# Performance work log

Measured on AMD Instinct MI355X. Metric: run time of the kernel, lower is better.

## Reference

```python
import jax, jax.numpy as jnp
import numpy as np

B, D_IN, P, H, E, K, NS, OUT = 4096, 512, 1024, 2048, 8, 2, 2, 29
HS = H * NS  # shared-expert intermediate size


def setup_inputs() -> dict:
    key = jax.random.key(0)
    ks = jax.random.split(key, 20)
    g = lambda i, shape, fan: jax.random.normal(ks[i], shape, jnp.float32) * (1.0 / np.sqrt(fan))
    return {
        "x": jax.random.normal(ks[0], (B, D_IN), jnp.float32),
        # input projection
        "Wproj": g(1, (D_IN, P), D_IN), "bproj": jnp.zeros((P,), jnp.float32),
        # router (Tutel top gate: linear, no bias)
        "Wg": g(2, (P, E), P),
        # fine experts (grouped FFN with fc1/fc2 bias)
        "W1": g(3, (E, P, H), P), "b1": jnp.zeros((E, H), jnp.float32),
        "W2": g(4, (E, H, P), H), "b2": jnp.zeros((E, P), jnp.float32),
        # shared experts: DeepseekV3MLP (SwiGLU with bias)
        "sg_w": g(5, (P, HS), P), "sg_b": jnp.zeros((HS,), jnp.float32),
        "su_w": g(6, (P, HS), P), "su_b": jnp.zeros((HS,), jnp.float32),
        "sd_w": g(7, (HS, P), HS), "sd_b": jnp.zeros((P,), jnp.float32),
        # output MLP + head
        "m1_w": g(8, (P, H), P), "m1_b": jnp.zeros((H,), jnp.float32),
        "m2_w": g(9, (H, H), H), "m2_b": jnp.zeros((H,), jnp.float32),
        "head_w": g(10, (H, OUT), H), "head_b": jnp.zeros((OUT,), jnp.float32),
    }


def reference(x, Wproj, bproj, Wg, W1, b1, W2, b2,
              sg_w, sg_b, su_w, su_b, sd_w, sd_b,
              m1_w, m1_b, m2_w, m2_b, head_w, head_b):
    silu = jax.nn.silu
    # input projection  [B, P]
    p = x @ Wproj + bproj

    # --- Tutel-style top-k gating (inference: gate_noise = 0, normalize=True) ---
    probs = jax.nn.softmax(p @ Wg, axis=-1)               # [B, E]
    top_vals, top_idx = jax.lax.top_k(probs, K)           # [B, K]
    gates = top_vals / jnp.sum(top_vals, axis=-1, keepdims=True)
    # combine weights as dense [B, E] (zero for non-selected experts)
    combine = jnp.zeros((p.shape[0], E), p.dtype).at[
        jnp.arange(p.shape[0])[:, None], top_idx].add(gates)

    # --- grouped-GEMM experts (ffn with fc1/fc2 bias, silu) ---
    h = silu(jnp.einsum('bp,eph->beh', p, W1) + b1)       # [B, E, H]
    eo = jnp.einsum('beh,ehp->bep', h, W2) + b2           # [B, E, P]
    moe_out = jnp.einsum('be,bep->bp', combine, eo)       # weighted combine

    # --- shared experts: SwiGLU MLP on residual stream ---
    shared = (silu(p @ sg_w + sg_b) * (p @ su_w + su_b)) @ sd_w + sd_b
    combined = moe_out + shared

    # --- output MLP + head ---
    hid = silu(combined @ m1_w + m1_b) @ m2_w + m2_b
    return hid @ head_w + head_b
```

## Files before the change

kernel.cpp:

```cpp
#include <hip/hip_runtime.h>
#include <hip/hip_bf16.h>
#include <cstdint>

typedef unsigned short us;
typedef __attribute__((ext_vector_type(4))) float f32x4;
typedef __attribute__((ext_vector_type(8))) short bf16x8;
typedef __attribute__((ext_vector_type(4))) short s16x4;
typedef __attribute__((ext_vector_type(8))) short s16x8;

__device__ __forceinline__ float b2f(us s){
  union { float f; unsigned u; } x; x.u = ((unsigned)s) << 16; return x.f;
}
__device__ __forceinline__ us f2b(float f){
  union { float f; unsigned u; } x; x.f = f;
  unsigned r = x.u + 0x7FFFu + ((x.u >> 16) & 1u);
  return (us)(r >> 16);
}

#define GLDS16(gp, lp) __builtin_amdgcn_global_load_lds( \
    (const __attribute__((address_space(1))) void*)(gp), \
    (__attribute__((address_space(3))) void*)(lp), 16, 0, 0)

__global__ void detect_kernel(const unsigned* __restrict__ xw, int* __restrict__ flag){
  __shared__ int cnt;
  if (threadIdx.x == 0) cnt = 0;
  __syncthreads();
  int c = 0;
  for (int i = threadIdx.x; i < 1024; i += 256){
    const unsigned e = (xw[i] >> 7) & 0xFF;
    if (e >= 100 && e <= 140) ++c;
  }
  atomicAdd(&cnt, c);
  __syncthreads();
  if (threadIdx.x == 0) *flag = (cnt < 512) ? 1 : 0;
}

template<bool OUT_BF16, bool SILU, bool MULG>
__global__ __launch_bounds__(256, 2)
void gemm_plain(const us* __restrict__ A, int lda,
                const us* __restrict__ BT, int ldb,
                void* __restrict__ Cout, int ldc,
                const us* __restrict__ bias,
                const us* __restrict__ mulg,
                int M, int N, int K, int Nvalid)
{
  __shared__ us As[128*32];
  __shared__ us Bs[128*32];
  const int bm = blockIdx.y * 128, bn = blockIdx.x * 128;
  const int tid = threadIdx.x, wave = tid >> 6, lane = tid & 63;
  const int llo = lane & 15, lhi = lane >> 4;

  const us* aP[2]; const us* bP[2]; us* lA[2]; us* lB[2];
#pragma unroll
  for (int s = 0; s < 2; ++s){
    const int chunk = s*256 + wave*64 + lane;
    const int r = chunk >> 2, cc = chunk & 3;
    aP[s] = A  + (size_t)(bm + r) * lda + cc*8;
    bP[s] = BT + (size_t)(bn + r) * ldb + cc*8;
    lA[s] = As + (size_t)(s*256 + wave*64) * 8;
    lB[s] = Bs + (size_t)(s*256 + wave*64) * 8;
  }

  f32x4 acc[4][4] = {};
  const int waveM = (wave >> 1) * 64, waveN = (wave & 1) * 64;

  for (int k0 = 0; k0 < K; k0 += 32){
    GLDS16(aP[0] + k0, lA[0]);
    GLDS16(aP[1] + k0, lA[1]);
    GLDS16(bP[0] + k0, lB[0]);
    GLDS16(bP[1] + k0, lB[1]);
    __syncthreads();
    bf16x8 af[4], bv[4];
#pragma unroll
    for (int t = 0; t < 4; ++t){
      af[t] = *reinterpret_cast<const bf16x8*>(As + (waveM + t*16 + llo)*32 + lhi*8);
      bv[t] = *reinterpret_cast<const bf16x8*>(Bs + (waveN + t*16 + llo)*32 + lhi*8);
    }
#pragma unroll
    for (int mt = 0; mt < 4; ++mt)
#pragma unroll
      for (int nt = 0; nt < 4; ++nt)
        acc[mt][nt] = __builtin_amdgcn_mfma_f32_16x16x32_bf16(af[mt], bv[nt], acc[mt][nt], 0, 0, 0);
    __syncthreads();
  }

#pragma unroll
  for (int nt = 0; nt < 4; ++nt){
    const int col = bn + waveN + nt*16 + llo;
    float bb = 0.f;
    if (bias && col < Nvalid) bb = b2f(bias[col]);
#pragma unroll
    for (int mt = 0; mt < 4; ++mt){
      const int row0 = bm + waveM + mt*16 + lhi*4;
#pragma unroll
      for (int r = 0; r < 4; ++r){
        if (col < Nvalid){
          float v = acc[mt][nt][r] + bb;
          if (SILU) v = v / (1.f + __expf(-v));
          if (MULG) v *= b2f(mulg[(size_t)(row0 + r) * ldc + col]);
          if (OUT_BF16) ((us*)Cout)[(size_t)(row0 + r) * ldc + col] = f2b(v);
          else          ((float*)Cout)[(size_t)(row0 + r) * ldc + col] = v;
        }
      }
    }
  }
}

template<bool OUT_BF16, bool SILU>
__global__ __launch_bounds__(256, 2)
void gemm_group(const us* __restrict__ Abase, int lda,
                const int* __restrict__ rowmap,
                const int* __restrict__ offsets,
                const us* __restrict__ BTbase,
                void* __restrict__ Cout, int ldc,
                const us* __restrict__ biasbase,
                int N, int K)
{
  const int e   = blockIdx.z;
  const int off = offsets[e];
  const int Te  = offsets[e + 1] - off;
  const int bmL = blockIdx.y * 128;
  if (bmL >= Te) return;

  __shared__ us As[128*32];
  __shared__ us Bs[128*32];
  const us* BT   = BTbase  + (size_t)e * N * K;
  const us* bias = biasbase + (size_t)e * N;
  const int bn = blockIdx.x * 128;
  const int tid = threadIdx.x, wave = tid >> 6, lane = tid & 63;
  const int llo = lane & 15, lhi = lane >> 4;

  const us* aP[2]; const us* bP[2]; us* lA[2]; us* lB[2];
#pragma unroll
  for (int s = 0; s < 2; ++s){
    const int chunk = s*256 + wave*64 + lane;
    const int r = chunk >> 2, cc = chunk & 3;
    int pos = off + bmL + r; if (pos > 8191) pos = 8191;
    const int arow = rowmap ? rowmap[pos] : pos;
    aP[s] = Abase + (size_t)arow * lda + cc*8;
    bP[s] = BT + (size_t)(bn + r) * K + cc*8;
    lA[s] = As + (size_t)(s*256 + wave*64) * 8;
    lB[s] = Bs + (size_t)(s*256 + wave*64) * 8;
  }

  f32x4 acc[4][4] = {};
  const int waveM = (wave >> 1) * 64, waveN = (wave & 1) * 64;

  for (int k0 = 0; k0 < K; k0 += 32){
    GLDS16(aP[0] + k0, lA[0]);
    GLDS16(aP[1] + k0, lA[1]);
    GLDS16(bP[0] + k0, lB[0]);
    GLDS16(bP[1] + k0, lB[1]);
    __syncthreads();
    bf16x8 af[4], bv[4];
#pragma unroll
    for (int t = 0; t < 4; ++t){
      af[t] = *reinterpret_cast<const bf16x8*>(As + (waveM + t*16 + llo)*32 + lhi*8);
      bv[t] = *reinterpret_cast<const bf16x8*>(Bs + (waveN + t*16 + llo)*32 + lhi*8);
    }
#pragma unroll
    for (int mt = 0; mt < 4; ++mt)
#pragma unroll
      for (int nt = 0; nt < 4; ++nt)
        acc[mt][nt] = __builtin_amdgcn_mfma_f32_16x16x32_bf16(af[mt], bv[nt], acc[mt][nt], 0, 0, 0);
    __syncthreads();
  }

#pragma unroll
  for (int nt = 0; nt < 4; ++nt){
    const int col = bn + waveN + nt*16 + llo;
    const float bb = b2f(bias[col]);
#pragma unroll
    for (int mt = 0; mt < 4; ++mt){
      const int localBase = bmL + waveM + mt*16 + lhi*4;
#pragma unroll
      for (int r = 0; r < 4; ++r){
        const int local = localBase + r;
        if (local < Te){
          float v = acc[mt][nt][r] + bb;
          if (SILU) v = v / (1.f + __expf(-v));
          const size_t row = (size_t)(off + local);
          if (OUT_BF16) ((us*)Cout)[row * ldc + col] = f2b(v);
          else          ((float*)Cout)[row * ldc + col] = v;
        }
      }
    }
  }
}

__global__ __launch_bounds__(256, 2)
void gemm_head(const us* __restrict__ A, const us* __restrict__ BT,
               float* __restrict__ Cpart)
{
  __shared__ us As[128*32];
  __shared__ us Bs[128*32];
  const int bm = blockIdx.y * 128;
  const int koff = blockIdx.z * 256;
  const int tid = threadIdx.x, wave = tid >> 6, lane = tid & 63;
  const int llo = lane & 15, lhi = lane >> 4;

  const us* aP[2]; const us* bP[2]; us* lA[2]; us* lB[2];
#pragma unroll
  for (int s = 0; s < 2; ++s){
    const int chunk = s*256 + wave*64 + lane;
    const int r = chunk >> 2, cc = chunk & 3;
    aP[s] = A  + (size_t)(bm + r) * 2048 + koff + cc*8;
    bP[s] = BT + (size_t)r * 2048 + koff + cc*8;
    lA[s] = As + (size_t)(s*256 + wave*64) * 8;
    lB[s] = Bs + (size_t)(s*256 + wave*64) * 8;
  }

  f32x4 acc[4][4] = {};
  const int waveM = (wave >> 1) * 64, waveN = (wave & 1) * 64;

  for (int k0 = 0; k0 < 256; k0 += 32){
    GLDS16(aP[0] + k0, lA[0]);
    GLDS16(aP[1] + k0, lA[1]);
    GLDS16(bP[0] + k0, lB[0]);
    GLDS16(bP[1] + k0, lB[1]);
    __syncthreads();
    bf16x8 af[4], bv[4];
#pragma unroll
    for (int t = 0; t < 4; ++t){
      af[t] = *reinterpret_cast<const bf16x8*>(As + (waveM + t*16 + llo)*32 + lhi*8);
      bv[t] = *reinterpret_cast<const bf16x8*>(Bs + (waveN + t*16 + llo)*32 + lhi*8);
    }
#pragma unroll
    for (int mt = 0; mt < 4; ++mt)
#pragma unroll
      for (int nt = 0; nt < 4; ++nt)
        acc[mt][nt] = __builtin_amdgcn_mfma_f32_16x16x32_bf16(af[mt], bv[nt], acc[mt][nt], 0, 0, 0);
    __syncthreads();
  }

  float* out = Cpart + (size_t)blockIdx.z * 4096 * 32;
#pragma unroll
  for (int nt = 0; nt < 4; ++nt){
    const int col = waveN + nt*16 + llo;
    if (col >= 29) continue;
#pragma unroll
    for (int mt = 0; mt < 4; ++mt){
      const int row0 = bm + waveM + mt*16 + lhi*4;
#pragma unroll
      for (int r = 0; r < 4; ++r)
        out[(size_t)(row0 + r) * 32 + col] = acc[mt][nt][r];
    }
  }
}

__global__ void reduce_head(const float* __restrict__ part, const us* __restrict__ bias,
                            void* __restrict__ dst, const int* __restrict__ flag){
  const int i = blockIdx.x * 256 + threadIdx.x;
  if (i >= 4096*29) return;
  const int t = i / 29, c = i - t * 29;
  float s = b2f(bias[c]);
#pragma unroll
  for (int z = 0; z < 8; ++z) s += part[((size_t)z * 4096 + t) * 32 + c];
  if (*flag) ((float*)dst)[i] = s;
  else       ((us*)dst)[i] = f2b(s);
}

__global__ void transpose_any(const void* __restrict__ src_, us* __restrict__ dst,
                              int R, int C, long long smat, long long dmat,
                              const int* __restrict__ flag)
{
  const int f32 = *flag;
  dst += (size_t)blockIdx.z * dmat;
  __shared__ us tile[32][33];
  const int c0 = blockIdx.x * 32, r0 = blockIdx.y * 32;
  const int tx = threadIdx.x & 31, ty = threadIdx.x >> 5;
#pragma unroll
  for (int i = 0; i < 4; ++i){
    const int r = r0 + ty + i*8, c = c0 + tx;
    const size_t idx = (size_t)blockIdx.z * smat + (size_t)r * C + c;
    us v = 0;
    if (c < C){
      if (f32) v = f2b(((const float*)src_)[idx]);
      else     v = ((const us*)src_)[idx];
    }
    tile[ty + i*8][tx] = v;
  }
  __syncthreads();
#pragma unroll
  for (int i = 0; i < 4; ++i){
    const int dr = c0 + ty + i*8;
    dst[(size_t)dr * R + r0 + tx] = tile[tx][ty + i*8];
  }
}

__global__ void cvt_any_bf(const void* __restrict__ src, us* __restrict__ dst, int n,
                           const int* __restrict__ flag){
  const int i = (blockIdx.x * 256 + threadIdx.x) * 4;
  if (i >= n) return;
  s16x4 o;
  if (*flag){
    f32x4 v = *reinterpret_cast<const f32x4*>((const float*)src + i);
#pragma unroll
    for (int k = 0; k < 4; ++k) o[k] = (short)f2b(v[k]);
  } else {
    o = *reinterpret_cast<const s16x4*>((const us*)src + i);
  }
  *reinterpret_cast<s16x4*>(dst + i) = o;
}

__global__ void compose_router(const void* __restrict__ Wproj, const void* __restrict__ Wg,
                               float* __restrict__ M, const int* __restrict__ flag)
{
  const int f32 = *flag;
  const int wave = threadIdx.x >> 6, lane = threadIdx.x & 63;
  const int d = blockIdx.x * 4 + wave;
  float acc[8] = {0,0,0,0,0,0,0,0};
  for (int n = lane; n < 1024; n += 64){
    float wp;
    if (f32) wp = ((const float*)Wproj)[(size_t)d * 1024 + n];
    else     wp = b2f(((const us*)Wproj)[(size_t)d * 1024 + n]);
    if (f32){
      const float* wg = (const float*)Wg + (size_t)n * 8;
#pragma unroll
      for (int e = 0; e < 8; ++e) acc[e] += wp * wg[e];
    } else {
      const s16x8 wg = *reinterpret_cast<const s16x8*>((const us*)Wg + (size_t)n * 8);
#pragma unroll
      for (int e = 0; e < 8; ++e) acc[e] += wp * b2f((us)wg[e]);
    }
  }
#pragma unroll
  for (int e = 0; e < 8; ++e){
    float v = acc[e];
    for (int off = 32; off > 0; off >>= 1) v += __shfl_down(v, off);
    if (lane == 0) M[(size_t)d * 8 + e] = v;
  }
}

__global__ void router2(const void* __restrict__ x, const float* __restrict__ M,
                        int* __restrict__ eidx, float* __restrict__ gates,
                        const int* __restrict__ flag)
{
  const int f32 = *flag;
  const int wave = threadIdx.x >> 6, lane = threadIdx.x & 63;
  const int t = blockIdx.x * 4 + wave;
  float l[8] = {0,0,0,0,0,0,0,0};
  for (int d = lane; d < 512; d += 64){
    float xv;
    if (f32) xv = ((const float*)x)[(size_t)t * 512 + d];
    else     xv = b2f(((const us*)x)[(size_t)t * 512 + d]);
    const float* mr = M + (size_t)d * 8;
#pragma unroll
    for (int e = 0; e < 8; ++e) l[e] += xv * mr[e];
  }
#pragma unroll
  for (int e = 0; e < 8; ++e){
    float v = l[e];
    for (int off = 32; off > 0; off >>= 1) v += __shfl_down(v, off);
    l[e] = v;
  }
  if (lane == 0){
    int e0 = 0; float v0 = l[0];
#pragma unroll
    for (int e = 1; e < 8; ++e) if (l[e] > v0){ v0 = l[e]; e0 = e; }
    int e1 = (e0 == 0) ? 1 : 0; float v1 = l[e1];
#pragma unroll
    for (int e = 0; e < 8; ++e) if (e != e0 && l[e] > v1){ v1 = l[e]; e1 = e; }
    const float g1 = 1.f / (1.f + __expf(v0 - v1));
    eidx[t*2] = e0;  eidx[t*2+1] = e1;
    gates[t*2] = 1.f - g1; gates[t*2+1] = g1;
  }
}

__global__ void hist_kernel(const int* __restrict__ eidx, int* __restrict__ counts){
  __shared__ int lh[8];
  if (threadIdx.x < 8) lh[threadIdx.x] = 0;
  __syncthreads();
  const int i = blockIdx.x * 256 + threadIdx.x;
  atomicAdd(&lh[eidx[i]], 1);
  __syncthreads();
  if (threadIdx.x < 8) atomicAdd(&counts[threadIdx.x], lh[threadIdx.x]);
}

__global__ void scan_kernel(const int* __restrict__ counts, int* __restrict__ offsets){
  if (threadIdx.x == 0){
    int s = 0;
    for (int e = 0; e < 8; ++e){ offsets[e] = s; s += counts[e]; }
    offsets[8] = s;
  }
}

__global__ void fill_kernel(const int* __restrict__ eidx, const int* __restrict__ offsets,
                            int* __restrict__ fillg, int* __restrict__ pos_tk,
                            int* __restrict__ tok_of_pos){
  __shared__ int lh[8];
  __shared__ int lbase[8];
  if (threadIdx.x < 8) lh[threadIdx.x] = 0;
  __syncthreads();
  const int i = blockIdx.x * 256 + threadIdx.x;
  const int e = eidx[i];
  const int r = atomicAdd(&lh[e], 1);
  __syncthreads();
  if (threadIdx.x < 8) lbase[threadIdx.x] = atomicAdd(&fillg[threadIdx.x], lh[threadIdx.x]);
  __syncthreads();
  const int pos = offsets[e] + lbase[e] + r;
  pos_tk[i] = pos;
  tok_of_pos[pos] = i >> 1;
}

__global__ void combine_kernel(const float* __restrict__ eo, const float* __restrict__ shr,
                               const int* __restrict__ pos_tk, const float* __restrict__ gates,
                               us* __restrict__ comb){
  const int t = blockIdx.x;
  const int c = threadIdx.x * 4;
  const int p0 = pos_tk[t*2], p1 = pos_tk[t*2+1];
  const float g0 = gates[t*2], g1 = gates[t*2+1];
  f32x4 a = *reinterpret_cast<const f32x4*>(eo + (size_t)p0 * 1024 + c);
  f32x4 b = *reinterpret_cast<const f32x4*>(eo + (size_t)p1 * 1024 + c);
  f32x4 s = *reinterpret_cast<const f32x4*>(shr + (size_t)t * 1024 + c);
  s16x4 o;
#pragma unroll
  for (int k = 0; k < 4; ++k) o[k] = (short)f2b(g0 * a[k] + g1 * b[k] + s[k]);
  *reinterpret_cast<s16x4*>(comb + (size_t)t * 1024 + c) = o;
}

extern "C" void kernel_launch(void* const* d_in, const int* in_sizes, int n_in,
                              void* d_out, int out_size, void* d_ws, size_t ws_size,
                              hipStream_t stream)
{
  const void* x      = d_in[0];
  const void* Wproj  = d_in[1];
  const us*   bproj  = (const us*)d_in[2];
  const void* Wg     = d_in[3];
  const void* W1     = d_in[4];
  const us*   b1     = (const us*)d_in[5];
  const void* W2     = d_in[6];
  const us*   b2     = (const us*)d_in[7];
  const void* sg_w   = d_in[8];
  const us*   sg_b   = (const us*)d_in[9];
  const void* su_w   = d_in[10];
  const us*   su_b   = (const us*)d_in[11];
  const void* sd_w   = d_in[12];
  const us*   sd_b   = (const us*)d_in[13];
  const void* m1_w   = d_in[14];
  const us*   m1_b   = (const us*)d_in[15];
  const void* m2_w   = d_in[16];
  const us*   m2_b   = (const us*)d_in[17];
  const void* head_w = d_in[18];
  const us*   head_b = (const us*)d_in[19];

  char* ws = (char*)d_ws;
  size_t off = 0;
  auto take = [&](size_t bytes) -> char* {
    char* p = ws + off; off += (bytes + 255) & ~(size_t)255; return p;
  };
  us* wprojT = (us*)take(1024ULL*512*2);
  us* w1T    = (us*)take(8ULL*2048*1024*2);
  us* w2T    = (us*)take(8ULL*1024*2048*2);
  us* sgT    = (us*)take(4096ULL*1024*2);
  us* suT    = (us*)take(4096ULL*1024*2);
  us* sdT    = (us*)take(1024ULL*4096*2);
  us* m1T    = (us*)take(2048ULL*1024*2);
  us* m2T    = (us*)take(2048ULL*2048*2);
  us* headT  = (us*)take(128ULL*2048*2);
  us* xb     = (us*)take(4096ULL*512*2);
  us* pbf    = (us*)take(4096ULL*1024*2);
  float* Mrt = (float*)take(512ULL*8*4);
  char* bufA = take(33554432);
  char* bufB = take(33554432);
  char* bufC = take(33554432);
  float* shrF  = (float*)take(4096ULL*1024*4);
  float* houtP = (float*)take(8ULL*4096*32*4);
  int* ctrl   = (int*)take(256);
  int* eidx   = (int*)take(8192*4);
  float* gbuf = (float*)take(8192*4);
  int* postk  = (int*)take(8192*4);
  int* tokpos = (int*)take(8192*4);
  int* counts  = ctrl;
  int* fill    = ctrl + 8;
  int* offs    = ctrl + 16;
  int* dflag   = ctrl + 28;

  us* comb = (us*)bufC;
  us* hid1 = (us*)(bufC + 8388608);
  us* hid2 = (us*)bufA;

  const dim3 T(256);
  const us* nomul = nullptr;

  detect_kernel<<<dim3(1), T, 0, stream>>>((const unsigned*)x, dflag);

  hipMemsetAsync(ctrl, 0, 64, stream);
  compose_router<<<dim3(128), T, 0, stream>>>(Wproj, Wg, Mrt, dflag);
  router2<<<dim3(1024), T, 0, stream>>>(x, Mrt, eidx, gbuf, dflag);
  hist_kernel<<<dim3(32), T, 0, stream>>>(eidx, counts);
  scan_kernel<<<dim3(1), dim3(64), 0, stream>>>(counts, offs);
  fill_kernel<<<dim3(32), T, 0, stream>>>(eidx, offs, fill, postk, tokpos);

  transpose_any<<<dim3(32, 16, 1), T, 0, stream>>>(Wproj, wprojT, 512, 1024, 0, 0, dflag);
  transpose_any<<<dim3(64, 32, 8), T, 0, stream>>>(W1, w1T, 1024, 2048, 1024LL*2048, 2048LL*1024, dflag);
  transpose_any<<<dim3(32, 64, 8), T, 0, stream>>>(W2, w2T, 2048, 1024, 2048LL*1024, 1024LL*2048, dflag);
  transpose_any<<<dim3(128, 32, 1), T, 0, stream>>>(sg_w, sgT, 1024, 4096, 0, 0, dflag);
  transpose_any<<<dim3(128, 32, 1), T, 0, stream>>>(su_w, suT, 1024, 4096, 0, 0, dflag);
  transpose_any<<<dim3(32, 128, 1), T, 0, stream>>>(sd_w, sdT, 4096, 1024, 0, 0, dflag);
  transpose_any<<<dim3(64, 32, 1), T, 0, stream>>>(m1_w, m1T, 1024, 2048, 0, 0, dflag);
  transpose_any<<<dim3(64, 64, 1), T, 0, stream>>>(m2_w, m2T, 2048, 2048, 0, 0, dflag);
  transpose_any<<<dim3(4, 64, 1), T, 0, stream>>>(head_w, headT, 2048, 29, 0, 0, dflag);

  cvt_any_bf<<<dim3(2048), T, 0, stream>>>(x, xb, 4096*512, dflag);
  gemm_plain<true,false,false><<<dim3(8, 32), T, 0, stream>>>(xb, 512, wprojT, 512, pbf, 1024, bproj, nomul, 4096, 1024, 512, 1024);

  gemm_plain<true,true ,false><<<dim3(32, 32), T, 0, stream>>>(pbf, 1024, sgT, 1024, bufA, 4096, sg_b, nomul, 4096, 4096, 1024, 4096);
  gemm_plain<true,false,true ><<<dim3(32, 32), T, 0, stream>>>(pbf, 1024, suT, 1024, bufC, 4096, su_b, (const us*)bufA, 4096, 4096, 1024, 4096);
  gemm_plain<false,false,false><<<dim3(8, 32), T, 0, stream>>>((us*)bufC, 4096, sdT, 4096, shrF, 1024, sd_b, nomul, 4096, 1024, 4096, 1024);

  gemm_group<true,true ><<<dim3(16, 64, 8), T, 0, stream>>>(pbf, 1024, tokpos, offs, w1T, bufA, 2048, b1, 2048, 1024);
  gemm_group<false,false><<<dim3(8, 64, 8), T, 0, stream>>>((us*)bufA, 2048, nullptr, offs, w2T, bufB, 1024, b2, 1024, 2048);
  combine_kernel<<<dim3(4096), T, 0, stream>>>((float*)bufB, shrF, postk, gbuf, comb);

  gemm_plain<true,true ,false><<<dim3(16, 32), T, 0, stream>>>(comb, 1024, m1T, 1024, hid1, 2048, m1_b, nomul, 4096, 2048, 1024, 2048);
  gemm_plain<true,false,false><<<dim3(16, 32), T, 0, stream>>>(hid1, 2048, m2T, 2048, hid2, 2048, m2_b, nomul, 4096, 2048, 2048, 2048);
  gemm_head<<<dim3(1, 32, 8), T, 0, stream>>>(hid2, headT, houtP);
  reduce_head<<<dim3(464), T, 0, stream>>>(houtP, head_b, d_out, dflag);

  (void)in_sizes; (void)n_in; (void)out_size; (void)ws_size;
}
```

Measured before the change: 792.9 us.

## Fuse shared-expert gate and up GEMMs and add XCD-aware block swizzle

Adds gemm_sgsu, one kernel that computes both the gate and up projections of the shared SwiGLU MLP from a single A tile and applies silu(g)*u in the epilogue. This removes one GEMM launch, a reload of the activation tile, and a full bf16 intermediate write and read through bufA. It also adds an XCD-aware block-index swizzle to the plain GEMMs so neighbouring tiles land on the same XCD for better L2 reuse. The fused kernel doubles the accumulator registers, which may cause spills or lower occupancy under launch_bounds(256,2).

```diff
diff --git a/kernel.cpp b/kernel.cpp
--- a/kernel.cpp
+++ b/kernel.cpp
@@ -21,6 +21,16 @@
     (const __attribute__((address_space(1))) void*)(gp), \
     (__attribute__((address_space(3))) void*)(lp), 16, 0, 0)
 
+__device__ __forceinline__ void xcd_swizzle(int& bm, int& bn){
+  const int gx = gridDim.x;
+  if (gridDim.y == 32 && (gx & 1) == 0 && gx >= 8){
+    const int lin = blockIdx.y * gx + blockIdx.x;
+    const int xcd = lin & 7, r = lin >> 3;
+    bm = (xcd & 3) * 8 + (r & 7);
+    bn = (xcd >> 2) * (gx >> 1) + (r >> 3);
+  } else { bm = blockIdx.y; bn = blockIdx.x; }
+}
+
 __global__ void detect_kernel(const unsigned* __restrict__ xw, int* __restrict__ flag){
   __shared__ int cnt;
   if (threadIdx.x == 0) cnt = 0;
@@ -35,18 +45,18 @@
   if (threadIdx.x == 0) *flag = (cnt < 512) ? 1 : 0;
 }
 
-template<bool OUT_BF16, bool SILU, bool MULG>
+template<bool OUT_BF16, bool SILU>
 __global__ __launch_bounds__(256, 2)
 void gemm_plain(const us* __restrict__ A, int lda,
                 const us* __restrict__ BT, int ldb,
                 void* __restrict__ Cout, int ldc,
                 const us* __restrict__ bias,
-                const us* __restrict__ mulg,
                 int M, int N, int K, int Nvalid)
 {
   __shared__ us As[128*32];
   __shared__ us Bs[128*32];
-  const int bm = blockIdx.y * 128, bn = blockIdx.x * 128;
+  int bmi, bni; xcd_swizzle(bmi, bni);
+  const int bm = bmi * 128, bn = bni * 128;
   const int tid = threadIdx.x, wave = tid >> 6, lane = tid & 63;
   const int llo = lane & 15, lhi = lane >> 4;
 
@@ -97,10 +107,83 @@
         if (col < Nvalid){
           float v = acc[mt][nt][r] + bb;
           if (SILU) v = v / (1.f + __expf(-v));
-          if (MULG) v *= b2f(mulg[(size_t)(row0 + r) * ldc + col]);
           if (OUT_BF16) ((us*)Cout)[(size_t)(row0 + r) * ldc + col] = f2b(v);
           else          ((float*)Cout)[(size_t)(row0 + r) * ldc + col] = v;
         }
+      }
+    }
+  }
+}
+
+__global__ __launch_bounds__(256, 2)
+void gemm_sgsu(const us* __restrict__ A, const us* __restrict__ B1T,
+               const us* __restrict__ B2T, const us* __restrict__ bias1,
+               const us* __restrict__ bias2, us* __restrict__ Cout)
+{
+  __shared__ us As[128*32];
+  __shared__ us B1s[128*32];
+  __shared__ us B2s[128*32];
+  int bmi, bni; xcd_swizzle(bmi, bni);
+  const int bm = bmi * 128, bn = bni * 128;
+  const int tid = threadIdx.x, wave = tid >> 6, lane = tid & 63;
+  const int llo = lane & 15, lhi = lane >> 4;
+
+  const us* aP[2]; const us* b1P[2]; const us* b2P[2];
+  us* lA[2]; us* lB1[2]; us* lB2[2];
+#pragma unroll
+  for (int s = 0; s < 2; ++s){
+    const int chunk = s*256 + wave*64 + lane;
+    const int r = chunk >> 2, cc = chunk & 3;
+    aP[s]  = A   + (size_t)(bm + r) * 1024 + cc*8;
+    b1P[s] = B1T + (size_t)(bn + r) * 1024 + cc*8;
+    b2P[s] = B2T + (size_t)(bn + r) * 1024 + cc*8;
+    lA[s]  = As  + (size_t)(s*256 + wave*64) * 8;
+    lB1[s] = B1s + (size_t)(s*256 + wave*64) * 8;
+    lB2[s] = B2s + (size_t)(s*256 + wave*64) * 8;
+  }
+
+  f32x4 acc1[4][4] = {};
+  f32x4 acc2[4][4] = {};
+  const int waveM = (wave >> 1) * 64, waveN = (wave & 1) * 64;
+
+  for (int k0 = 0; k0 < 1024; k0 += 32){
+    GLDS16(aP[0] + k0, lA[0]);
+    GLDS16(aP[1] + k0, lA[1]);
+    GLDS16(b1P[0] + k0, lB1[0]);
+    GLDS16(b1P[1] + k0, lB1[1]);
+    GLDS16(b2P[0] + k0, lB2[0]);
+    GLDS16(b2P[1] + k0, lB2[1]);
+    __syncthreads();
+    bf16x8 af[4], b1v[4], b2v[4];
+#pragma unroll
+    for (int t = 0; t < 4; ++t){
+      af[t]  = *reinterpret_cast<const bf16x8*>(As  + (waveM + t*16 + llo)*32 + lhi*8);
+      b1v[t] = *reinterpret_cast<const bf16x8*>(B1s + (waveN + t*16 + llo)*32 + lhi*8);
+      b2v[t] = *reinterpret_cast<const bf16x8*>(B2s + (waveN + t*16 + llo)*32 + lhi*8);
+    }
+#pragma unroll
+    for (int mt = 0; mt < 4; ++mt)
+#pragma unroll
+      for (int nt = 0; nt < 4; ++nt){
+        acc1[mt][nt] = __builtin_amdgcn_mfma_f32_16x16x32_bf16(af[mt], b1v[nt], acc1[mt][nt], 0, 0, 0);
+        acc2[mt][nt] = __builtin_amdgcn_mfma_f32_16x16x32_bf16(af[mt], b2v[nt], acc2[mt][nt], 0, 0, 0);
+      }
+    __syncthreads();
+  }
+
+#pragma unroll
+  for (int nt = 0; nt < 4; ++nt){
+    const int col = bn + waveN + nt*16 + llo;
+    const float bb1 = b2f(bias1[col]);
+    const float bb2 = b2f(bias2[col]);
+#pragma unroll
+    for (int mt = 0; mt < 4; ++mt){
+      const int row0 = bm + waveM + mt*16 + lhi*4;
+#pragma unroll
+      for (int r = 0; r < 4; ++r){
+        const float g = acc1[mt][nt][r] + bb1;
+        const float v = (g / (1.f + __expf(-g))) * (acc2[mt][nt][r] + bb2);
+        Cout[(size_t)(row0 + r) * 4096 + col] = f2b(v);
       }
     }
   }
@@ -481,7 +564,6 @@
   us* hid2 = (us*)bufA;
 
   const dim3 T(256);
-  const us* nomul = nullptr;
 
   detect_kernel<<<dim3(1), T, 0, stream>>>((const unsigned*)x, dflag);
 
@@ -503,18 +585,17 @@
   transpose_any<<<dim3(4, 64, 1), T, 0, stream>>>(head_w, headT, 2048, 29, 0, 0, dflag);
 
   cvt_any_bf<<<dim3(2048), T, 0, stream>>>(x, xb, 4096*512, dflag);
-  gemm_plain<true,false,false><<<dim3(8, 32), T, 0, stream>>>(xb, 512, wprojT, 512, pbf, 1024, bproj, nomul, 4096, 1024, 512, 1024);
-
-  gemm_plain<true,true ,false><<<dim3(32, 32), T, 0, stream>>>(pbf, 1024, sgT, 1024, bufA, 4096, sg_b, nomul, 4096, 4096, 1024, 4096);
-  gemm_plain<true,false,true ><<<dim3(32, 32), T, 0, stream>>>(pbf, 1024, suT, 1024, bufC, 4096, su_b, (const us*)bufA, 4096, 4096, 1024, 4096);
-  gemm_plain<false,false,false><<<dim3(8, 32), T, 0, stream>>>((us*)bufC, 4096, sdT, 4096, shrF, 1024, sd_b, nomul, 4096, 1024, 4096, 1024);
+  gemm_plain<true,false><<<dim3(8, 32), T, 0, stream>>>(xb, 512, wprojT, 512, pbf, 1024, bproj, 4096, 1024, 512, 1024);
+
+  gemm_sgsu<<<dim3(32, 32), T, 0, stream>>>(pbf, sgT, suT, sg_b, su_b, (us*)bufC);
+  gemm_plain<false,false><<<dim3(8, 32), T, 0, stream>>>((us*)bufC, 4096, sdT, 4096, shrF, 1024, sd_b, 4096, 1024, 4096, 1024);
 
   gemm_group<true,true ><<<dim3(16, 64, 8), T, 0, stream>>>(pbf, 1024, tokpos, offs, w1T, bufA, 2048, b1, 2048, 1024);
   gemm_group<false,false><<<dim3(8, 64, 8), T, 0, stream>>>((us*)bufA, 2048, nullptr, offs, w2T, bufB, 1024, b2, 1024, 2048);
   combine_kernel<<<dim3(4096), T, 0, stream>>>((float*)bufB, shrF, postk, gbuf, comb);
 
-  gemm_plain<true,true ,false><<<dim3(16, 32), T, 0, stream>>>(comb, 1024, m1T, 1024, hid1, 2048, m1_b, nomul, 4096, 2048, 1024, 2048);
-  gemm_plain<true,false,false><<<dim3(16, 32), T, 0, stream>>>(hid1, 2048, m2T, 2048, hid2, 2048, m2_b, nomul, 4096, 2048, 2048, 2048);
+  gemm_plain<true,true ><<<dim3(16, 32), T, 0, stream>>>(comb, 1024, m1T, 1024, hid1, 2048, m1_b, 4096, 2048, 1024, 2048);
+  gemm_plain<true,false><<<dim3(16, 32), T, 0, stream>>>(hid1, 2048, m2T, 2048, hid2, 2048, m2_b, 4096, 2048, 2048, 2048);
   gemm_head<<<dim3(1, 32, 8), T, 0, stream>>>(hid2, headT, houtP);
   reduce_head<<<dim3(464), T, 0, stream>>>(houtP, head_b, d_out, dflag);
 
```

Measured after the change: 759.6 us. 4.2% less time.
